# Performance work log

Hardware: AMD Instinct MI355X
Metric: run time of the kernel (lower is better)

## Reference

```python
import jax, jax.numpy as jnp
import numpy as np

B, N, D, H, E = 4, 2048, 512, 8, 512   # batch, seq, d_model, heads, dpb_embedding
D1 = 2 * D                              # expand_ratio * d_model (multiple of H)
HD = D1 // H                            # head dim for v/u space
GAMMA = 0.999


def _srms(x):
    # SimpleRMSNorm: x / (||x|| * d^-0.5 + eps)
    return x / (jnp.sqrt(jnp.mean(jnp.square(x), axis=-1, keepdims=True)) + 1e-8)


def setup_inputs() -> dict:
    key = jax.random.key(0)
    ks = jax.random.split(key, 10)
    s = 0.02

    def lin(k, i, o):
        kw, kb = jax.random.split(k)
        return (jax.random.normal(kw, (i, o), jnp.float32) * s,
                jax.random.normal(kb, (o,), jnp.float32) * s)

    Wu, bu = lin(ks[0], D, D1)
    Wv, bv = lin(ks[1], D, D1)
    Wo, bo = lin(ks[2], D1, D)
    Wp, bp = lin(ks[3], 1, E)        # DPB pos_proj: scalar position -> dpb_dim
    W1, b1 = lin(ks[4], E, E)
    W2, b2 = lin(ks[5], E, E)
    W3, b3 = lin(ks[6], E, E)
    Wz, bz = lin(ks[7], E, H * HD)   # DPB out: dpb_dim -> h*head_dim
    x = jax.random.normal(ks[8], (B, N, D), jnp.float32)
    return dict(x=x, Wu=Wu, bu=bu, Wv=Wv, bv=bv, Wo=Wo, bo=bo,
                Wp=Wp, bp=bp, W1=W1, b1=b1, W2=W2, b2=b2, W3=W3, b3=b3,
                Wz=Wz, bz=bz)


def reference(x, Wu, bu, Wv, bv, Wo, bo, Wp, bp, W1, b1, W2, b2, W3, b3, Wz, bz):
    shortcut = x                       # token_shift_type=-1, resi_param=False
    xn = _srms(x)                      # pre_norm = SimpleRMSNorm(d_model)
    u = jax.nn.silu(xn @ Wu + bu)      # b n d1
    v = jax.nn.silu(xn @ Wv + bv)      # b n d1
    b, n, _ = x.shape
    v = v.reshape(b, n, H, HD).transpose(0, 2, 1, 3)   # b h n d

    # --- DPB (Rpe MLP) on positions [0, 1, ..., n-1]; row 0 is the zero lag ---
    pos = jnp.arange(0, n, dtype=x.dtype).reshape(n, 1)  # par_type=1
    hcf = pos @ Wp + bp
    for W, bb in ((W1, b1), (W2, b2), (W3, b3)):         # non-residual layers
        hcf = jax.nn.relu(_srms(hcf)) @ W + bb
    coef = jax.nn.relu(_srms(hcf)) @ Wz + bz             # n, h*d
    coef = coef.reshape(n, H, HD).transpose(1, 0, 2)     # h n d
    zero = coef[:, :1]                                   # h 1 d  (lag 0)
    posc = coef[:, 1:]                                   # h n-1 d (lags 1..n-1)

    # fixed exponential decay gamma^i on positive lags (use_decay=True)
    decay = GAMMA ** jnp.arange(1, n, dtype=x.dtype)[None, :, None]
    # causal: negative lags are zero; rfft zero-pads to 2n
    a = jnp.concatenate([zero, decay * posc, zero], axis=1)  # h, n+1, d

    # --- causal Toeplitz matmul as circular conv of length 2n ---
    m = 2 * n
    fv = jnp.fft.rfft(v, m, axis=2)           # b h m/2+1 d
    fa = jnp.fft.rfft(a, m, axis=1)[None]     # 1 h m/2+1 d
    out = jnp.fft.irfft(fv * fa, m, axis=2)[:, :, :n]  # b h n d

    out = out.transpose(0, 2, 1, 3).reshape(b, n, H * HD)  # b n d1
    out = u * out                               # u-gating
    return out @ Wo + bo + shortcut             # output proj + residual
```

## Files before the change

kernel.cpp:

```cpp
#include <hip/hip_runtime.h>
#include <hip/hip_bf16.h>
#include <math.h>

using bf16 = __hip_bfloat16;
typedef short bf16x8 __attribute__((ext_vector_type(8)));
typedef float f32x4 __attribute__((ext_vector_type(4)));

#define GAMMA_LOG2 (-0.0014434688536725045f)

union Bf16Bits { bf16 h; unsigned short s; };
union VecU { uint4 q; unsigned short s[8]; };

__device__ inline unsigned short bf16_bits(float z)
{
    Bf16Bits u;
    u.h = __float2bfloat16(z);
    return u.s;
}

__device__ inline unsigned int packbf2(float a, float b)
{
    return (unsigned int)bf16_bits(a) | ((unsigned int)bf16_bits(b) << 16);
}

__device__ __forceinline__ void async_copy16(unsigned short* lds, const bf16* g)
{
    __builtin_amdgcn_global_load_lds(
        (const __attribute__((address_space(1))) unsigned int*)(const void*)g,
        (__attribute__((address_space(3))) unsigned int*)(void*)lds,
        16, 0, 0);
}

struct PrepArgs {
    const float* src[3];
    bf16* dst[3];
    int R[3];
    int C[3];
    int pfx[4];
};

__global__ void k_prep(PrepArgs pa)
{
    __shared__ float tile[32][33];
    int bid = blockIdx.x;
    int seg = 0;
    while (bid >= pa.pfx[seg + 1]) ++seg;
    int local = bid - pa.pfx[seg];
    int R = pa.R[seg], C = pa.C[seg];
    int ctiles = C >> 5;
    int c0 = (local % ctiles) * 32, r0 = (local / ctiles) * 32;
    const float* in = pa.src[seg];
    bf16* out = pa.dst[seg];
    int tx = threadIdx.x & 31, ty = threadIdx.x >> 5;
#pragma unroll
    for (int i = 0; i < 4; ++i) {
        int r = r0 + ty + 8 * i;
        tile[ty + 8 * i][tx] = in[(size_t)r * C + c0 + tx];
    }
    __syncthreads();
#pragma unroll
    for (int i = 0; i < 4; ++i) {
        int cc = c0 + ty + 8 * i, rr = r0 + tx;
        out[(size_t)cc * R + rr] = __float2bfloat16(tile[tx][ty + 8 * i]);
    }
}

__global__ void k_prep_mlp(const float* __restrict__ W1, const float* __restrict__ W2,
                           const float* __restrict__ W3, const float* __restrict__ Wz,
                           bf16* __restrict__ Wf)
{
    int g = blockIdx.x * 256 + threadIdx.x;
    int unit = g >> 15;
    int idx = g & 32767;
    int lane = idx & 63;
    int nj = (idx >> 6) & 7;
    int ks = (idx >> 9) & 15;
    int wc = idx >> 13;
    int lm = lane & 15, lq = lane >> 4;
    int k0 = ks * 32 + lq * 8;
    const float* src;
    int N, o;
    if (unit < 3) {
        src = (unit == 0) ? W1 : (unit == 1) ? W2 : W3;
        N = 512;
        o = wc * 128 + nj * 16 + lm;
    } else {
        src = Wz;
        N = 1024;
        o = (unit - 3) * 512 + wc * 128 + nj * 16 + lm;
    }
    VecU v;
#pragma unroll
    for (int j = 0; j < 8; ++j)
        v.s[j] = bf16_bits(src[(size_t)(k0 + j) * N + o]);
    *(uint4*)(void*)(Wf + (size_t)g * 8) = v.q;
}

__global__ void k_transpose_a(const bf16* __restrict__ ab, bf16* __restrict__ atb)
{
    __shared__ unsigned short tile[64][65];
    const int t = threadIdx.x;
    int c0 = blockIdx.x * 64, r0 = blockIdx.y * 64;
#pragma unroll
    for (int it = 0; it < 2; ++it) {
        int r = it * 32 + (t >> 3), cc = (t & 7) * 8;
        VecU v;
        v.q = *(const uint4*)(const void*)(ab + (size_t)(r0 + r) * 1024 + c0 + cc);
#pragma unroll
        for (int i = 0; i < 8; ++i) tile[r][cc + i] = v.s[i];
    }
    __syncthreads();
#pragma unroll
    for (int it = 0; it < 2; ++it) {
        int c = it * 32 + (t >> 3), rr = (t & 7) * 8;
        VecU v;
#pragma unroll
        for (int i = 0; i < 8; ++i) v.s[i] = tile[rr + i][c];
        *(uint4*)(void*)(atb + (size_t)(c0 + c) * 2048 + r0 + rr) = v.q;
    }
}

__global__ void k_gate_transpose(const bf16* __restrict__ ud1t, const bf16* __restrict__ uv,
                                 bf16* __restrict__ out)
{
    __shared__ unsigned short tile[64][65];
    const int b = blockIdx.z;
    const int t = threadIdx.x;
    int c0 = blockIdx.x * 64, t0 = blockIdx.y * 64;
#pragma unroll
    for (int it = 0; it < 2; ++it) {
        int r = it * 32 + (t >> 3), cc = (t & 7) * 8;
        VecU v;
        v.q = *(const uint4*)(const void*)(ud1t + ((size_t)b * 1024 + c0 + r) * 2048 + t0 + cc);
#pragma unroll
        for (int i = 0; i < 8; ++i) tile[r][cc + i] = v.s[i];
    }
    __syncthreads();
#pragma unroll
    for (int it = 0; it < 2; ++it) {
        int tt = it * 32 + (t >> 3), cc = (t & 7) * 8;
        VecU vu;
        vu.q = *(const uint4*)(const void*)(uv + ((size_t)b * 2048 + t0 + tt) * 2048 + c0 + cc);
        VecU vo;
#pragma unroll
        for (int i = 0; i < 8; ++i) {
            Bf16Bits cv, uu;
            cv.s = tile[cc + i][tt];
            uu.s = vu.s[i];
            vo.s[i] = bf16_bits(__bfloat162float(cv.h) * __bfloat162float(uu.h));
        }
        *(uint4*)(void*)(out + ((size_t)b * 2048 + t0 + tt) * 1024 + c0 + cc) = vo.q;
    }
}

__global__ void k_rms_x(const float* __restrict__ x, bf16* __restrict__ xn)
{
    int row = blockIdx.x, t = threadIdx.x;
    const float* xr = x + (size_t)row * 512;
    float a = xr[t], b = xr[t + 256];
    float v = a * a + b * b;
#pragma unroll
    for (int m = 32; m >= 1; m >>= 1) v += __shfl_xor(v, m, 64);
    __shared__ float ws[4];
    if ((t & 63) == 0) ws[t >> 6] = v;
    __syncthreads();
    float tot = ws[0] + ws[1] + ws[2] + ws[3];
    float s = 1.f / (sqrtf(tot * (1.f / 512.f)) + 1e-8f);
    bf16* o = xn + (size_t)row * 512;
    o[t] = __float2bfloat16(a * s);
    o[t + 256] = __float2bfloat16(b * s);
}

__global__ __launch_bounds__(1024, 1) void k_mlp(
    const float* __restrict__ Wp, const float* __restrict__ bp,
    const bf16* __restrict__ Wf,
    const float* __restrict__ b1, const float* __restrict__ b2,
    const float* __restrict__ b3, const float* __restrict__ bz,
    bf16* __restrict__ ab)
{
    __shared__ unsigned short X[32][520];
    __shared__ float sq2[32][33];
    __shared__ float red[16][32];
    __shared__ float scale[32];

    const int tid = threadIdx.x, lane = tid & 63, w = tid >> 6;
    const int lm = lane & 15, lq = lane >> 4;
    const int posBase = blockIdx.x * 32;

    {
        const int r = tid >> 5;
        const int cb = tid & 31;
        const int c0 = cb * 16;
        float vals[16];
        float ssq = 0.f;
        const float fp = (float)(posBase + r);
#pragma unroll
        for (int e = 0; e < 16; ++e) {
            float z = fp * Wp[c0 + e] + bp[c0 + e];
            vals[e] = z;
            ssq += z * z;
        }
        sq2[r][cb] = ssq;
        __syncthreads();
        float tot = 0.f;
#pragma unroll
        for (int i = 0; i < 32; ++i) tot += sq2[r][i];
        float s = 1.f / (sqrtf(tot * (1.f / 512.f)) + 1e-8f);
        unsigned int* xrow = (unsigned int*)&X[r][c0];
#pragma unroll
        for (int e = 0; e < 8; ++e)
            xrow[e] = packbf2(fmaxf(vals[2 * e] * s, 0.f), fmaxf(vals[2 * e + 1] * s, 0.f));
        __syncthreads();
    }

    const int wc = w >> 2, njb = (w & 3) * 2;

    auto layer_mm = [&](const bf16* Wu_, f32x4 (&acc)[2][2]) {
        const bf16* base = Wu_ + (size_t)wc * 65536 + (size_t)njb * 512 + (size_t)lane * 8;
        bf16x8 bufB[4][2];
#pragma unroll
        for (int d = 0; d < 3; ++d)
#pragma unroll
            for (int nj = 0; nj < 2; ++nj)
                bufB[d][nj] = *(const bf16x8*)(const void*)(base + d * 4096 + nj * 512);
#pragma unroll
        for (int ks = 0; ks < 16; ++ks) {
            const int cb = ks & 3;
            if (ks < 13) {
                const int pf = (ks + 3) & 3;
#pragma unroll
                for (int nj = 0; nj < 2; ++nj)
                    bufB[pf][nj] = *(const bf16x8*)(const void*)(base + (ks + 3) * 4096 + nj * 512);
            }
            bf16x8 af0 = *(const bf16x8*)(const void*)&X[lm][ks * 32 + lq * 8];
            bf16x8 af1 = *(const bf16x8*)(const void*)&X[16 + lm][ks * 32 + lq * 8];
#pragma unroll
            for (int nj = 0; nj < 2; ++nj) {
                acc[0][nj] = __builtin_amdgcn_mfma_f32_16x16x32_bf16(af0, bufB[cb][nj], acc[0][nj], 0, 0, 0);
                acc[1][nj] = __builtin_amdgcn_mfma_f32_16x16x32_bf16(af1, bufB[cb][nj], acc[1][nj], 0, 0, 0);
            }
        }
    };

    const float* bs[3] = {b1, b2, b3};
    for (int l = 0; l < 3; ++l) {
        f32x4 acc[2][2];
#pragma unroll
        for (int mi = 0; mi < 2; ++mi)
#pragma unroll
            for (int i = 0; i < 2; ++i) acc[mi][i] = (f32x4){0.f, 0.f, 0.f, 0.f};
        layer_mm(Wf + (size_t)l * 262144, acc);
#pragma unroll
        for (int mi = 0; mi < 2; ++mi)
#pragma unroll
            for (int nj = 0; nj < 2; ++nj) {
                float bb = bs[l][w * 32 + nj * 16 + lm];
#pragma unroll
                for (int r = 0; r < 4; ++r) acc[mi][nj][r] += bb;
            }
        float pr[2][4] = {{0.f, 0.f, 0.f, 0.f}, {0.f, 0.f, 0.f, 0.f}};
#pragma unroll
        for (int mi = 0; mi < 2; ++mi)
#pragma unroll
            for (int nj = 0; nj < 2; ++nj)
#pragma unroll
                for (int r = 0; r < 4; ++r) pr[mi][r] += acc[mi][nj][r] * acc[mi][nj][r];
#pragma unroll
        for (int m = 1; m < 16; m <<= 1)
#pragma unroll
            for (int mi = 0; mi < 2; ++mi)
#pragma unroll
                for (int r = 0; r < 4; ++r) pr[mi][r] += __shfl_xor(pr[mi][r], m);
        if (lm == 0)
#pragma unroll
            for (int mi = 0; mi < 2; ++mi)
#pragma unroll
                for (int r = 0; r < 4; ++r) red[w][mi * 16 + lq * 4 + r] = pr[mi][r];
        __syncthreads();
        if (tid < 32) {
            float tot = 0.f;
#pragma unroll
            for (int wv = 0; wv < 16; ++wv) tot += red[wv][tid];
            scale[tid] = 1.f / (sqrtf(tot * (1.f / 512.f)) + 1e-8f);
        }
        __syncthreads();
#pragma unroll
        for (int mi = 0; mi < 2; ++mi)
#pragma unroll
            for (int nj = 0; nj < 2; ++nj) {
                int col = w * 32 + nj * 16 + lm;
#pragma unroll
                for (int r = 0; r < 4; ++r) {
                    int row = mi * 16 + lq * 4 + r;
                    float z = fmaxf(acc[mi][nj][r] * scale[row], 0.f);
                    *(unsigned short*)&X[row][col] = bf16_bits(z);
                }
            }
        __syncthreads();
    }

#pragma unroll
    for (int h = 0; h < 2; ++h) {
        f32x4 acc[2][2];
#pragma unroll
        for (int mi = 0; mi < 2; ++mi)
#pragma unroll
            for (int i = 0; i < 2; ++i) acc[mi][i] = (f32x4){0.f, 0.f, 0.f, 0.f};
        layer_mm(Wf + (size_t)(3 + h) * 262144, acc);
#pragma unroll
        for (int mi = 0; mi < 2; ++mi)
#pragma unroll
            for (int nj = 0; nj < 2; ++nj) {
                int col = h * 512 + w * 32 + nj * 16 + lm;
                float bb = bz[col];
#pragma unroll
                for (int r = 0; r < 4; ++r) {
                    int pos = posBase + mi * 16 + lq * 4 + r;
                    float z = (acc[mi][nj][r] + bb) * exp2f((float)pos * GAMMA_LOG2);
                    ab[(size_t)pos * 1024 + col] = __float2bfloat16(z);
                }
            }
    }
}

__global__ __launch_bounds__(256, 4) void k_uv(
    const bf16* __restrict__ A, const bf16* __restrict__ Bt,
    const float* __restrict__ bu, const float* __restrict__ bv,
    bf16* __restrict__ uvb, bf16* __restrict__ vtb)
{
    __shared__ unsigned short AB[2][2][128 * 32];

    const int tid = threadIdx.x, lane = tid & 63, w = tid >> 6;
    const int lm = lane & 15, lq = lane >> 4;
    const int gid = blockIdx.x;
    const int wm = (w >> 1) * 64, wn = (w & 1) * 64;
    const long rowBase = (long)(gid & 63) * 128, colBase = (long)(gid >> 6) * 128;

    const int srow = tid >> 2;
    const int sqz  = (tid & 3) ^ ((srow >> 1) & 3);
    const bf16* gA  = A  + (rowBase + srow) * 512 + sqz * 8;
    const bf16* gB  = Bt + (colBase + srow) * 512 + sqz * 8;
    const bf16* gA2 = gA + (size_t)64 * 512;
    const bf16* gB2 = gB + (size_t)64 * 512;
    const int ls0 = w * 512;
    const int ls1 = 2048 + w * 512;

    const int rdA = ((wm + lm) * 4 + (lq ^ ((lm >> 1) & 3))) * 8;
    const int rdB = ((wn + lm) * 4 + (lq ^ ((lm >> 1) & 3))) * 8;

    f32x4 acc[4][4];
    f32x4 zz = {0.f, 0.f, 0.f, 0.f};
#pragma unroll
    for (int i = 0; i < 4; ++i)
#pragma unroll
        for (int j = 0; j < 4; ++j) acc[i][j] = zz;

    async_copy16(&AB[0][0][ls0], gA);
    async_copy16(&AB[0][0][ls1], gA2);
    async_copy16(&AB[0][1][ls0], gB);
    async_copy16(&AB[0][1][ls1], gB2);
    __syncthreads();

#pragma unroll
    for (int t = 0; t < 16; ++t) {
        const int cur = t & 1;
        if (t < 15) {
            const int kk = (t + 1) * 32;
            async_copy16(&AB[cur ^ 1][0][ls0], gA + kk);
            async_copy16(&AB[cur ^ 1][0][ls1], gA2 + kk);
            async_copy16(&AB[cur ^ 1][1][ls0], gB + kk);
            async_copy16(&AB[cur ^ 1][1][ls1], gB2 + kk);
        }
        bf16x8 af[4], bfr[4];
#pragma unroll
        for (int mi = 0; mi < 4; ++mi)
            af[mi] = *(const bf16x8*)(const void*)&AB[cur][0][rdA + mi * 512];
#pragma unroll
        for (int nj = 0; nj < 4; ++nj)
            bfr[nj] = *(const bf16x8*)(const void*)&AB[cur][1][rdB + nj * 512];
#pragma unroll
        for (int mi = 0; mi < 4; ++mi)
#pragma unroll
            for (int nj = 0; nj < 4; ++nj)
                acc[mi][nj] = __builtin_amdgcn_mfma_f32_16x16x32_bf16(af[mi], bfr[nj], acc[mi][nj], 0, 0, 0);
        if (t < 15) __syncthreads();
    }

    const bool vhalf = colBase >= 1024;
    if (!vhalf) {
#pragma unroll
        for (int mi = 0; mi < 4; ++mi)
#pragma unroll
            for (int nj = 0; nj < 4; ++nj) {
                long col = colBase + wn + nj * 16 + lm;
                float bb = bu[col];
                long row0 = rowBase + wm + mi * 16 + lq * 4;
#pragma unroll
                for (int r = 0; r < 4; ++r) {
                    float z = acc[mi][nj][r] + bb;
                    z = z / (1.f + __expf(-z));
                    uvb[(size_t)(row0 + r) * 2048 + col] = __float2bfloat16(z);
                }
            }
    } else {
        __syncthreads();
        unsigned short* sh = &AB[0][0][0];
#pragma unroll
        for (int mi = 0; mi < 4; ++mi)
#pragma unroll
            for (int nj = 0; nj < 4; ++nj) {
                int c_local = wn + nj * 16 + lm;
                float bb = bv[colBase - 1024 + c_local];
                int t_local = wm + mi * 16 + lq * 4;
                float zs[4];
#pragma unroll
                for (int r = 0; r < 4; ++r) {
                    float z = acc[mi][nj][r] + bb;
                    zs[r] = z / (1.f + __expf(-z));
                }
                int p = (t_local + 8 * c_local) & 127;
                uint2 o;
                o.x = packbf2(zs[0], zs[1]);
                o.y = packbf2(zs[2], zs[3]);
                *(uint2*)(void*)&sh[c_local * 128 + p] = o;
            }
        __syncthreads();
        const int b   = (int)(rowBase >> 11);
        const int tb0 = (int)(rowBase & 2047);
        const long cb = colBase - 1024;
        const int cl = tid >> 4;
        const int ch = tid & 15;
#pragma unroll
        for (int it = 0; it < 8; ++it) {
            int c_local = it * 16 + cl;
            int p = (ch * 8 + 8 * c_local) & 127;
            uint4 q = *(const uint4*)(const void*)&sh[c_local * 128 + p];
            *(uint4*)(void*)(vtb + ((size_t)b * 1024 + cb + c_local) * 2048 + tb0 + ch * 8) = q;
        }
    }
}

template <int BM, int BN, int WM, int WN>
__global__ __launch_bounds__(256, 2) void k_gemm_out(
    const bf16* __restrict__ A, const bf16* __restrict__ Bt,
    const float* __restrict__ bias0, const float* __restrict__ addsrc,
    float* __restrict__ outp, int M, int N, int K)
{
    constexpr int BK = 32, LDT = BK + 8;
    constexpr int MI = WM / 16, NJ = WN / 16;
    constexpr int WCOLS = BN / WN;
    __shared__ unsigned short As[BM * LDT];
    __shared__ unsigned short Bs[BN * LDT];
    const int tid = threadIdx.x;
    const int lane = tid & 63, w = tid >> 6;
    const int wm = (w / WCOLS) * WM, wn = (w % WCOLS) * WN;
    const int lm = lane & 15, lq = lane >> 4;
    const long rowBase = (long)blockIdx.x * BM, colBase = (long)blockIdx.y * BN;

    f32x4 acc[MI][NJ];
    f32x4 zz = {0.f, 0.f, 0.f, 0.f};
#pragma unroll
    for (int i = 0; i < MI; ++i)
#pragma unroll
        for (int j = 0; j < NJ; ++j) acc[i][j] = zz;

    for (int k0 = 0; k0 < K; k0 += BK) {
#pragma unroll
        for (int i = 0; i < BM / 64; ++i) {
            int idx = (i * 256 + tid) * 8;
            int r = idx >> 5, kk = idx & 31;
            *(uint4*)(void*)(As + r * LDT + kk) =
                *(const uint4*)(const void*)(A + (rowBase + r) * K + k0 + kk);
        }
#pragma unroll
        for (int i = 0; i < BN / 64; ++i) {
            int idx = (i * 256 + tid) * 8;
            int r = idx >> 5, kk = idx & 31;
            *(uint4*)(void*)(Bs + r * LDT + kk) =
                *(const uint4*)(const void*)(Bt + (colBase + r) * K + k0 + kk);
        }
        __syncthreads();
        bf16x8 af[MI], bfr[NJ];
#pragma unroll
        for (int mi = 0; mi < MI; ++mi)
            af[mi] = *(const bf16x8*)(const void*)(As + (wm + mi * 16 + lm) * LDT + lq * 8);
#pragma unroll
        for (int nj = 0; nj < NJ; ++nj)
            bfr[nj] = *(const bf16x8*)(const void*)(Bs + (wn + nj * 16 + lm) * LDT + lq * 8);
#pragma unroll
        for (int mi = 0; mi < MI; ++mi)
#pragma unroll
            for (int nj = 0; nj < NJ; ++nj)
                acc[mi][nj] = __builtin_amdgcn_mfma_f32_16x16x32_bf16(af[mi], bfr[nj], acc[mi][nj], 0, 0, 0);
        __syncthreads();
    }

#pragma unroll
    for (int mi = 0; mi < MI; ++mi)
#pragma unroll
        for (int nj = 0; nj < NJ; ++nj) {
            long col = colBase + wn + nj * 16 + lm;
#pragma unroll
            for (int r = 0; r < 4; ++r) {
                long row = rowBase + wm + mi * 16 + lq * 4 + r;
                size_t off = (size_t)row * N + col;
                outp[off] = acc[mi][nj][r] + bias0[col] + addsrc[off];
            }
        }
}

__global__ __launch_bounds__(256, 4) void k_conv_mfma(
    const bf16* __restrict__ vt, const bf16* __restrict__ at, bf16* __restrict__ ud1t)
{
    __shared__ unsigned short ash2[2][2068];
    __shared__ unsigned short vsh[4][3072];

    const int tid = threadIdx.x, lane = tid & 63, w = tid >> 6;
    const int c = blockIdx.x;

    {
        const unsigned short* asrc = (const unsigned short*)(at + (size_t)c * 2048);
        for (int i = tid; i < 2068; i += 256) {
#pragma unroll
            for (int k = 0; k < 2; ++k) {
                int src = 2047 - i - k;
                ash2[k][i] = (src >= 0) ? asrc[src] : (unsigned short)0;
            }
        }
    }
    {
        const bf16* vsrc = vt + ((size_t)w * 1024 + c) * 2048;
#pragma unroll
        for (int q = 0; q < 4; ++q) {
            int li = q * 64 + lane;
            int tile = li >> 1, hf = li & 1;
            *(uint4*)(void*)&vsh[w][tile * 24 + hf * 8] =
                *(const uint4*)(const void*)(vsrc + li * 8);
        }
    }
    __syncthreads();

    const int lm = lane & 15, lq = lane >> 4;
    const int h = lq >> 1, p0 = (lq & 1) * 8;
    const int kcopy = (lm + 1) & 1;
    const int base = 31 - 16 * h - lm + p0 - kcopy;
    const unsigned int* aw = (const unsigned int*)(void*)&ash2[kcopy][0] + (base >> 1);
    const unsigned short* vw = &vsh[w][0];

    f32x4 acc[8];
    f32x4 zz = {0.f, 0.f, 0.f, 0.f};
#pragma unroll
    for (int i = 0; i < 8; ++i) acc[i] = zz;
    const bf16x8 zfrag = (bf16x8)(short)0;

    for (int d2 = 0; d2 < 16; d2 += 2) {
        bf16x8 vf[8];
        const int tb = lm - d2 - h;
        {
            int T = tb > 0 ? tb : 0;
            bf16x8 f = *(const bf16x8*)(const void*)(vw + T * 24 + p0);
            vf[0] = (tb < 0) ? zfrag : f;
        }
#pragma unroll
        for (int dl = 1; dl < 8; ++dl)
            vf[dl] = *(const bf16x8*)(const void*)(vw + (dl * 16 + tb) * 24 + p0);

#pragma unroll
        for (int dt = 0; dt < 8; ++dt) {
            const int m16 = (63 - ((dt * 16 + d2) >> 1)) * 16;
            union { unsigned int u[4]; bf16x8 v; } af;
            af.u[0] = aw[m16 + 0];
            af.u[1] = aw[m16 + 1];
            af.u[2] = aw[m16 + 2];
            af.u[3] = aw[m16 + 3];
#pragma unroll
            for (int dl = 0; dl < 8 - dt; ++dl)
                acc[dt + dl] = __builtin_amdgcn_mfma_f32_16x16x32_bf16(af.v, vf[dl], acc[dt + dl], 0, 0, 0);
        }
    }

    __syncthreads();
    float* stg = (float*)(void*)((char*)(void*)&ash2[0][0] + w * 1024);
    bf16* dst = ud1t + ((size_t)w * 1024 + c) * 2048;
#pragma unroll
    for (int jg = 0; jg < 8; ++jg) {
        *(f32x4*)(void*)&stg[lm * 16 + lq * 4] = acc[jg];
        f32x4 vv = *(const f32x4*)(const void*)&stg[lane * 4];
        uint2 o;
        o.x = packbf2(vv.x, vv.y);
        o.y = packbf2(vv.z, vv.w);
        *(uint2*)(void*)(dst + jg * 256 + lane * 4) = o;
    }
}

extern "C" void kernel_launch(void* const* d_in, const int* in_sizes, int n_in,
                              void* d_out, int out_size, void* d_ws, size_t ws_size,
                              hipStream_t stream)
{
    const float* x  = (const float*)d_in[0];
    const float* Wu = (const float*)d_in[1];
    const float* bu = (const float*)d_in[2];
    const float* Wv = (const float*)d_in[3];
    const float* bv = (const float*)d_in[4];
    const float* Wo = (const float*)d_in[5];
    const float* bo = (const float*)d_in[6];
    const float* Wp = (const float*)d_in[7];
    const float* bp = (const float*)d_in[8];
    const float* W1 = (const float*)d_in[9];
    const float* b1 = (const float*)d_in[10];
    const float* W2 = (const float*)d_in[11];
    const float* b2 = (const float*)d_in[12];
    const float* W3 = (const float*)d_in[13];
    const float* b3 = (const float*)d_in[14];
    const float* Wz = (const float*)d_in[15];
    const float* bz = (const float*)d_in[16];

    char* p = (char*)d_ws;
    auto carve = [&](size_t bytes) { void* q = (void*)p; p += (bytes + 255) & ~(size_t)255; return q; };
    bf16*  xn   = (bf16*)carve((size_t)8192 * 512 * 2);
    bf16*  Wuvt = (bf16*)carve((size_t)2048 * 512 * 2);
    bf16*  Wot  = (bf16*)carve((size_t)512 * 1024 * 2);
    bf16*  Wf   = (bf16*)carve((size_t)5 * 262144 * 2);
    bf16*  uvb  = (bf16*)carve((size_t)8192 * 2048 * 2);
    bf16*  ud1  = (bf16*)carve((size_t)8192 * 1024 * 2);
    bf16*  ab   = (bf16*)carve((size_t)2048 * 1024 * 2);
    bf16*  vtb  = (bf16*)carve((size_t)4 * 1024 * 2048 * 2);
    bf16*  atb  = (bf16*)carve((size_t)1024 * 2048 * 2);
    bf16*  ud1t = (bf16*)carve((size_t)4 * 1024 * 2048 * 2);

    PrepArgs pa;
    const float* srcs[3] = {Wu, Wv, Wo};
    bf16* dsts[3] = {Wuvt, Wuvt + (size_t)1024 * 512, Wot};
    int Rs[3] = {512, 512, 1024};
    int Cs[3] = {1024, 1024, 512};
    int acc_t = 0;
    for (int i = 0; i < 3; ++i) {
        pa.src[i] = srcs[i]; pa.dst[i] = dsts[i]; pa.R[i] = Rs[i]; pa.C[i] = Cs[i];
        pa.pfx[i] = acc_t;
        acc_t += (Rs[i] / 32) * (Cs[i] / 32);
    }
    pa.pfx[3] = acc_t;
    k_prep<<<acc_t, 256, 0, stream>>>(pa);

    k_prep_mlp<<<640, 256, 0, stream>>>(W1, W2, W3, Wz, Wf);

    k_rms_x<<<8192, 256, 0, stream>>>(x, xn);

    k_mlp<<<64, 1024, 0, stream>>>(Wp, bp, Wf, b1, b2, b3, bz, ab);

    k_uv<<<1024, 256, 0, stream>>>(xn, Wuvt, bu, bv, uvb, vtb);

    k_transpose_a<<<dim3(16, 32), 256, 0, stream>>>(ab, atb);

    k_conv_mfma<<<dim3(1024), 256, 0, stream>>>(vtb, atb, ud1t);

    k_gate_transpose<<<dim3(16, 32, 4), 256, 0, stream>>>(ud1t, uvb, ud1);

    k_gemm_out<128, 128, 64, 64><<<dim3(64, 4), 256, 0, stream>>>(
        ud1, Wot, bo, x, (float*)d_out, 8192, 512, 1024);
}
```

Before: 232.7 us.

## Rewrite output GEMM with double-buffered async copies, swizzled LDS and smaller tiles

```diff
diff --git a/kernel.cpp b/kernel.cpp
--- a/kernel.cpp
+++ b/kernel.cpp
@@ -440,71 +440,77 @@
     }
 }
 
-template <int BM, int BN, int WM, int WN>
-__global__ __launch_bounds__(256, 2) void k_gemm_out(
+__global__ __launch_bounds__(256, 4) void k_gemm_out2(
     const bf16* __restrict__ A, const bf16* __restrict__ Bt,
     const float* __restrict__ bias0, const float* __restrict__ addsrc,
-    float* __restrict__ outp, int M, int N, int K)
-{
-    constexpr int BK = 32, LDT = BK + 8;
-    constexpr int MI = WM / 16, NJ = WN / 16;
-    constexpr int WCOLS = BN / WN;
-    __shared__ unsigned short As[BM * LDT];
-    __shared__ unsigned short Bs[BN * LDT];
-    const int tid = threadIdx.x;
-    const int lane = tid & 63, w = tid >> 6;
-    const int wm = (w / WCOLS) * WM, wn = (w % WCOLS) * WN;
+    float* __restrict__ outp)
+{
+    __shared__ unsigned short As[2][64 * 32];
+    __shared__ unsigned short Bs[2][128 * 32];
+
+    const int tid = threadIdx.x, lane = tid & 63, w = tid >> 6;
     const int lm = lane & 15, lq = lane >> 4;
-    const long rowBase = (long)blockIdx.x * BM, colBase = (long)blockIdx.y * BN;
-
-    f32x4 acc[MI][NJ];
+    const int wm = (w >> 1) * 32, wn = (w & 1) * 64;
+    const long rowBase = (long)blockIdx.x * 64, colBase = (long)blockIdx.y * 128;
+
+    const int srow = tid >> 2;
+    const int sqz  = (tid & 3) ^ ((srow >> 1) & 3);
+    const bf16* gA  = A  + (rowBase + srow) * 1024 + sqz * 8;
+    const bf16* gB  = Bt + (colBase + srow) * 1024 + sqz * 8;
+    const bf16* gB2 = gB + (size_t)64 * 1024;
+    const int lsA = w * 512;
+    const int lsB0 = w * 512, lsB1 = 2048 + w * 512;
+
+    const int rdA = ((wm + lm) * 4 + (lq ^ ((lm >> 1) & 3))) * 8;
+    const int rdB = ((wn + lm) * 4 + (lq ^ ((lm >> 1) & 3))) * 8;
+
+    f32x4 acc[2][4];
     f32x4 zz = {0.f, 0.f, 0.f, 0.f};
 #pragma unroll
-    for (int i = 0; i < MI; ++i)
-#pragma unroll
-        for (int j = 0; j < NJ; ++j) acc[i][j] = zz;
-
-    for (int k0 = 0; k0 < K; k0 += BK) {
-#pragma unroll
-        for (int i = 0; i < BM / 64; ++i) {
-            int idx = (i * 256 + tid) * 8;
-            int r = idx >> 5, kk = idx & 31;
-            *(uint4*)(void*)(As + r * LDT + kk) =
-                *(const uint4*)(const void*)(A + (rowBase + r) * K + k0 + kk);
-        }
-#pragma unroll
-        for (int i = 0; i < BN / 64; ++i) {
-            int idx = (i * 256 + tid) * 8;
-            int r = idx >> 5, kk = idx & 31;
-            *(uint4*)(void*)(Bs + r * LDT + kk) =
-                *(const uint4*)(const void*)(Bt + (colBase + r) * K + k0 + kk);
-        }
-        __syncthreads();
-        bf16x8 af[MI], bfr[NJ];
-#pragma unroll
-        for (int mi = 0; mi < MI; ++mi)
-            af[mi] = *(const bf16x8*)(const void*)(As + (wm + mi * 16 + lm) * LDT + lq * 8);
-#pragma unroll
-        for (int nj = 0; nj < NJ; ++nj)
-            bfr[nj] = *(const bf16x8*)(const void*)(Bs + (wn + nj * 16 + lm) * LDT + lq * 8);
-#pragma unroll
-        for (int mi = 0; mi < MI; ++mi)
-#pragma unroll
-            for (int nj = 0; nj < NJ; ++nj)
+    for (int i = 0; i < 2; ++i)
+#pragma unroll
+        for (int j = 0; j < 4; ++j) acc[i][j] = zz;
+
+    async_copy16(&As[0][lsA], gA);
+    async_copy16(&Bs[0][lsB0], gB);
+    async_copy16(&Bs[0][lsB1], gB2);
+    __syncthreads();
+
+#pragma unroll
+    for (int t = 0; t < 32; ++t) {
+        const int cur = t & 1;
+        if (t < 31) {
+            const int kk = (t + 1) * 32;
+            async_copy16(&As[cur ^ 1][lsA], gA + kk);
+            async_copy16(&Bs[cur ^ 1][lsB0], gB + kk);
+            async_copy16(&Bs[cur ^ 1][lsB1], gB2 + kk);
+        }
+        bf16x8 af[2], bfr[4];
+#pragma unroll
+        for (int mi = 0; mi < 2; ++mi)
+            af[mi] = *(const bf16x8*)(const void*)&As[cur][rdA + mi * 512];
+#pragma unroll
+        for (int nj = 0; nj < 4; ++nj)
+            bfr[nj] = *(const bf16x8*)(const void*)&Bs[cur][rdB + nj * 512];
+#pragma unroll
+        for (int mi = 0; mi < 2; ++mi)
+#pragma unroll
+            for (int nj = 0; nj < 4; ++nj)
                 acc[mi][nj] = __builtin_amdgcn_mfma_f32_16x16x32_bf16(af[mi], bfr[nj], acc[mi][nj], 0, 0, 0);
-        __syncthreads();
-    }
-
-#pragma unroll
-    for (int mi = 0; mi < MI; ++mi)
-#pragma unroll
-        for (int nj = 0; nj < NJ; ++nj) {
+        if (t < 31) __syncthreads();
+    }
+
+#pragma unroll
+    for (int mi = 0; mi < 2; ++mi)
+#pragma unroll
+        for (int nj = 0; nj < 4; ++nj) {
             long col = colBase + wn + nj * 16 + lm;
+            float bb = bias0[col];
 #pragma unroll
             for (int r = 0; r < 4; ++r) {
                 long row = rowBase + wm + mi * 16 + lq * 4 + r;
-                size_t off = (size_t)row * N + col;
-                outp[off] = acc[mi][nj][r] + bias0[col] + addsrc[off];
+                size_t off = (size_t)row * 512 + col;
+                outp[off] = acc[mi][nj][r] + bb + addsrc[off];
             }
         }
 }
@@ -656,6 +662,5 @@
 
     k_gate_transpose<<<dim3(16, 32, 4), 256, 0, stream>>>(ud1t, uvb, ud1);
 
-    k_gemm_out<128, 128, 64, 64><<<dim3(64, 4), 256, 0, stream>>>(
-        ud1, Wot, bo, x, (float*)d_out, 8192, 512, 1024);
-}
+    k_gemm_out2<<<dim3(128, 4), 256, 0, stream>>>(ud1, Wot, bo, x, (float*)d_out);
+}
```

Result: no change. 231.3 us (-0.6%).
